# Optimization experiments

Hardware: AMD Instinct MI355X
Metric: run time of the kernel (lower is better)

## Reference

```python
import jax, jax.numpy as jnp
import numpy as np

COMMITMENT_COST = 0.25


def setup_inputs() -> dict:
    key = jax.random.key(0)
    k1, k2 = jax.random.split(key)
    n_embeddings, embedding_dim = 1024, 256
    x = jax.random.normal(k1, (32, 2048, embedding_dim), dtype=jnp.float32)
    r = 1.0 / n_embeddings
    embedding = jax.random.uniform(k2, (n_embeddings, embedding_dim),
                                   dtype=jnp.float32, minval=-r, maxval=r)
    return {"x": x, "embedding": embedding}


def reference(x, embedding):
    M, D = embedding.shape
    # x is detached before flattening in the original quantize()
    x_flat = jax.lax.stop_gradient(x).reshape(-1, D)  # [N, D]
    distances = (jnp.sum(embedding * embedding, axis=1)
                 + jnp.sum(x_flat * x_flat, axis=1, keepdims=True)
                 - 2.0 * (x_flat @ embedding.T))  # [N, M]
    indices = jnp.argmin(distances, axis=-1)  # [N] int
    quantized = embedding[indices].reshape(x.shape)  # gather + view_as(x)
    # commitment loss: quantized is detached in the loss term
    e_latent_loss = jnp.mean(jnp.square(x - jax.lax.stop_gradient(quantized)))
    loss = COMMITMENT_COST * e_latent_loss
    return quantized, loss, indices
```

## Files before the change

kernel.cpp:

```cpp
#include <hip/hip_runtime.h>

#define N_ROWS   65536
#define D        256
#define D4       64
#define M        1024
#define LOSS_OFF 16777216
#define IDX_OFF  16777217
#define COMMIT_SCALE (0.25f / 16777216.0f)
#define E_SCALE  1024.0f
#define C_SCALE  0.001953125f

typedef _Float16 f16x8 __attribute__((ext_vector_type(8)));
typedef _Float16 f16x4 __attribute__((ext_vector_type(4)));
typedef float    f32x4 __attribute__((ext_vector_type(4)));

__device__ __forceinline__ float np_block128(const float* __restrict__ a, int l) {
    float r0 = __fmul_rn(a[l +   0], a[l +   0]);
    float r1 = __fmul_rn(a[l +  16], a[l +  16]);
    float r2 = __fmul_rn(a[l +  32], a[l +  32]);
    float r3 = __fmul_rn(a[l +  48], a[l +  48]);
    float r4 = __fmul_rn(a[l +  64], a[l +  64]);
    float r5 = __fmul_rn(a[l +  80], a[l +  80]);
    float r6 = __fmul_rn(a[l +  96], a[l +  96]);
    float r7 = __fmul_rn(a[l + 112], a[l + 112]);
    return __fadd_rn(__fadd_rn(__fadd_rn(r0, r1), __fadd_rn(r2, r3)),
                     __fadd_rn(__fadd_rn(r4, r5), __fadd_rn(r6, r7)));
}
__device__ __forceinline__ float np_reduce16(float v) {
    float s = __fadd_rn(v, __shfl_down(v, 8));
    s = __fadd_rn(s, __shfl_down(s, 4));
    s = __fadd_rn(s, __shfl_down(s, 2));
    s = __fadd_rn(s, __shfl_down(s, 1));
    return s;
}

__global__ __launch_bounds__(256) void norms_kernel(
    const float* __restrict__ x, const float* __restrict__ emb,
    float* __restrict__ bsq, float* __restrict__ esq,
    float* __restrict__ loss_slot) {
    const int tid = threadIdx.x;
    const int l = tid & 15, g = tid >> 4;
    const float* src;
    float* dst;
    if (blockIdx.x < 4096) {
        const int row = blockIdx.x * 16 + g;
        src = x + (size_t)row * D;
        dst = bsq + row;
    } else {
        const int row = (blockIdx.x - 4096) * 16 + g;
        src = emb + (size_t)row * D;
        dst = esq + row;
    }
    const float v0 = np_block128(src, l);
    const float v1 = np_block128(src + 128, l);
    const float t0 = np_reduce16(v0);
    const float t1 = np_reduce16(v1);
    if (l == 0) *dst = __fadd_rn(t0, t1);
    if (blockIdx.x == 0 && tid == 0) *loss_slot = 0.0f;
}

__global__ __launch_bounds__(256) void esplit_kernel(
    const float4* __restrict__ emb4,
    _Float16* __restrict__ e_hi, _Float16* __restrict__ e_mid) {
    const int f = blockIdx.x * 256 + threadIdx.x;
    float4 v = emb4[f];
    float a[4] = {v.x * E_SCALE, v.y * E_SCALE, v.z * E_SCALE, v.w * E_SCALE};
    f16x4 hi, mid;
    #pragma unroll
    for (int j = 0; j < 4; ++j) {
        _Float16 h = (_Float16)a[j];
        float r = __fsub_rn(a[j], (float)h);
        hi[j] = h;
        mid[j] = (_Float16)r;
    }
    *(f16x4*)&e_hi[f * 4]  = hi;
    *(f16x4*)&e_mid[f * 4] = mid;
}

__global__ __launch_bounds__(256, 2) void argmin_mfma_kernel(
    const float* __restrict__ x,
    const _Float16* __restrict__ e_hi, const _Float16* __restrict__ e_mid,
    const float* __restrict__ esq, const float* __restrict__ bsq,
    float* __restrict__ idx_out_f, int* __restrict__ idx_out_i) {
    __shared__ _Float16 bs[2][128 * 40];
    __shared__ float red_d[64][2];
    __shared__ int   red_i[64][2];

    const int tid = threadIdx.x;
    const int w = tid >> 6, lane = tid & 63;
    const int w_row = w >> 1, w_col = w & 1;
    const int lm = lane & 15, q = lane >> 4;
    const int row0 = blockIdx.x * 64;

    f16x8 a_hi[2][8], a_mid[2][8];
    #pragma unroll
    for (int fm = 0; fm < 2; ++fm) {
        const float* xr = x + (size_t)(row0 + w_row * 32 + fm * 16 + lm) * D + q * 8;
        #pragma unroll
        for (int kc = 0; kc < 8; ++kc) {
            float4 v0 = *(const float4*)(xr + kc * 32);
            float4 v1 = *(const float4*)(xr + kc * 32 + 4);
            float e[8] = {v0.x, v0.y, v0.z, v0.w, v1.x, v1.y, v1.z, v1.w};
            #pragma unroll
            for (int j = 0; j < 8; ++j) {
                _Float16 h = (_Float16)e[j];
                float r = __fsub_rn(e[j], (float)h);
                a_hi[fm][kc][j]  = h;
                a_mid[fm][kc][j] = (_Float16)r;
            }
        }
    }
    float bq[2][4];
    #pragma unroll
    for (int fm = 0; fm < 2; ++fm)
        #pragma unroll
        for (int r = 0; r < 4; ++r)
            bq[fm][r] = bsq[row0 + w_row * 32 + fm * 16 + q * 4 + r];

    float best[2][4] = {{3.0e38f, 3.0e38f, 3.0e38f, 3.0e38f},
                        {3.0e38f, 3.0e38f, 3.0e38f, 3.0e38f}};
    int bidx[2][4] = {{0, 0, 0, 0}, {0, 0, 0, 0}};

    const int sc = tid >> 1;
    const int sh = tid & 1;

    for (int jt = 0; jt < 8; ++jt) {
        const int j0 = jt * 128;
        f32x4 acc[2][4] = {};
        #pragma unroll
        for (int kc = 0; kc < 8; ++kc) {
            __syncthreads();
            const size_t gofs = (size_t)(j0 + sc) * D + kc * 32 + sh * 16;
            _Float16* dh = &bs[0][sc * 40 + sh * 16];
            _Float16* dm = &bs[1][sc * 40 + sh * 16];
            *(uint4*)(dh)     = *(const uint4*)(e_hi + gofs);
            *(uint4*)(dh + 8) = *(const uint4*)(e_hi + gofs + 8);
            *(uint4*)(dm)     = *(const uint4*)(e_mid + gofs);
            *(uint4*)(dm + 8) = *(const uint4*)(e_mid + gofs + 8);
            __syncthreads();
            f16x8 bh[4], bm[4];
            #pragma unroll
            for (int fn = 0; fn < 4; ++fn) {
                const int bo = (w_col * 64 + fn * 16 + lm) * 40 + q * 8;
                bh[fn] = *(const f16x8*)&bs[0][bo];
                bm[fn] = *(const f16x8*)&bs[1][bo];
            }
            #pragma unroll
            for (int fm = 0; fm < 2; ++fm)
                #pragma unroll
                for (int fn = 0; fn < 4; ++fn) {
                    acc[fm][fn] = __builtin_amdgcn_mfma_f32_16x16x32_f16(
                        a_hi[fm][kc], bh[fn], acc[fm][fn], 0, 0, 0);
                    acc[fm][fn] = __builtin_amdgcn_mfma_f32_16x16x32_f16(
                        a_mid[fm][kc], bh[fn], acc[fm][fn], 0, 0, 0);
                    acc[fm][fn] = __builtin_amdgcn_mfma_f32_16x16x32_f16(
                        a_hi[fm][kc], bm[fn], acc[fm][fn], 0, 0, 0);
                }
        }
        #pragma unroll
        for (int fn = 0; fn < 4; ++fn) {
            const int j = j0 + w_col * 64 + fn * 16 + lm;
            const float eq = esq[j];
            #pragma unroll
            for (int fm = 0; fm < 2; ++fm)
                #pragma unroll
                for (int r = 0; r < 4; ++r) {
                    const float d = __fsub_rn(__fadd_rn(eq, bq[fm][r]),
                                              acc[fm][fn][r] * C_SCALE);
                    if (d < best[fm][r]) { best[fm][r] = d; bidx[fm][r] = j; }
                }
        }
    }
    #pragma unroll
    for (int fm = 0; fm < 2; ++fm)
        #pragma unroll
        for (int r = 0; r < 4; ++r) {
            float d = best[fm][r]; int i = bidx[fm][r];
            #pragma unroll
            for (int mv = 1; mv <= 8; mv <<= 1) {
                const float d2 = __shfl_xor(d, mv, 64);
                const int   i2 = __shfl_xor(i, mv, 64);
                if (d2 < d || (d2 == d && i2 < i)) { d = d2; i = i2; }
            }
            best[fm][r] = d; bidx[fm][r] = i;
        }
    __syncthreads();
    if (lm == 0) {
        #pragma unroll
        for (int fm = 0; fm < 2; ++fm)
            #pragma unroll
            for (int r = 0; r < 4; ++r) {
                const int rl = w_row * 32 + fm * 16 + q * 4 + r;
                red_d[rl][w_col] = best[fm][r];
                red_i[rl][w_col] = bidx[fm][r];
            }
    }
    __syncthreads();
    if (tid < 64) {
        float d0 = red_d[tid][0]; int i0 = red_i[tid][0];
        const float d1 = red_d[tid][1]; const int i1 = red_i[tid][1];
        if (d1 < d0 || (d1 == d0 && i1 < i0)) { d0 = d1; i0 = i1; }
        idx_out_f[row0 + tid] = (float)i0;
        idx_out_i[row0 + tid] = i0;
    }
}

__global__ __launch_bounds__(256) void gather_loss_kernel(
    const float4* __restrict__ x4, const float4* __restrict__ emb4,
    const int* __restrict__ idx, float4* __restrict__ q4,
    float* __restrict__ loss_slot) {
    const int base = blockIdx.x * 256 + threadIdx.x;
    float acc = 0.0f;
    #pragma unroll
    for (int i = 0; i < 16; ++i) {
        const int f   = base + i * (1024 * 256);
        const int row = f >> 6;
        const int c4  = f & 63;
        const int e   = idx[row];
        float4 qv = emb4[e * D4 + c4];
        float4 xv = x4[f];
        q4[f] = qv;
        const float dx = xv.x - qv.x, dy = xv.y - qv.y;
        const float dz = xv.z - qv.z, dw = xv.w - qv.w;
        acc += dx * dx + dy * dy + dz * dz + dw * dw;
    }
    #pragma unroll
    for (int off = 32; off; off >>= 1) acc += __shfl_down(acc, off, 64);
    __shared__ float wsum[4];
    const int lane = threadIdx.x & 63, w = threadIdx.x >> 6;
    if (lane == 0) wsum[w] = acc;
    __syncthreads();
    if (threadIdx.x == 0) {
        atomicAdd(loss_slot, (wsum[0] + wsum[1] + wsum[2] + wsum[3]) * COMMIT_SCALE);
    }
}

extern "C" void kernel_launch(void* const* d_in, const int* in_sizes, int n_in,
                              void* d_out, int out_size, void* d_ws, size_t ws_size,
                              hipStream_t stream) {
    const float* x   = (const float*)d_in[0];
    const float* emb = (const float*)d_in[1];
    float* out = (float*)d_out;
    float*    bsq  = (float*)d_ws;
    float*    esq  = bsq + N_ROWS;
    int*      idx  = (int*)(esq + M);
    _Float16* e_hi = (_Float16*)(idx + N_ROWS);
    _Float16* e_mid = e_hi + (size_t)M * D;

    norms_kernel<<<4096 + M / 16, 256, 0, stream>>>(x, emb, bsq, esq,
                                                    out + LOSS_OFF);
    esplit_kernel<<<M * D / 4 / 256, 256, 0, stream>>>((const float4*)emb,
                                                       e_hi, e_mid);
    argmin_mfma_kernel<<<N_ROWS / 64, 256, 0, stream>>>(x, e_hi, e_mid,
                                                        esq, bsq,
                                                        out + IDX_OFF, idx);
    gather_loss_kernel<<<1024, 256, 0, stream>>>((const float4*)x,
                                                 (const float4*)emb, idx,
                                                 (float4*)out, out + LOSS_OFF);
}
```

Before: 253.5 us.

## Double-buffer codebook tiles via async global-to-LDS loads and stage norm rows in LDS

The fp16 hi/mid codebook split is now written in a kc-major tiled layout. This lets each 128-code by 32-dim tile be copied into LDS with contiguous global_load_lds DMA. The argmin kernel double-buffers these tiles and prefetches the next one while MFMAs run on the current one, which removes one barrier per step and the register round-trip of the staging copy. The norms kernel now loads 16 rows with coalesced float4 reads into padded shared memory before doing the same fixed-order reduction. Risks: the unpadded 32-half LDS row stride may cause bank conflicts, and correctness relies on the barrier waiting for the async LDS writes to complete.

```diff
diff --git a/kernel.cpp b/kernel.cpp
--- a/kernel.cpp
+++ b/kernel.cpp
@@ -13,6 +13,12 @@
 typedef _Float16 f16x8 __attribute__((ext_vector_type(8)));
 typedef _Float16 f16x4 __attribute__((ext_vector_type(4)));
 typedef float    f32x4 __attribute__((ext_vector_type(4)));
+
+__device__ __forceinline__ void async_copy16(const void* g, void* l) {
+    __builtin_amdgcn_global_load_lds(
+        (const __attribute__((address_space(1))) unsigned int*)g,
+        (__attribute__((address_space(3))) unsigned int*)l, 16, 0, 0);
+}
 
 __device__ __forceinline__ float np_block128(const float* __restrict__ a, int l) {
     float r0 = __fmul_rn(a[l +   0], a[l +   0]);
@@ -35,27 +41,37 @@
 }
 
 __global__ __launch_bounds__(256) void norms_kernel(
-    const float* __restrict__ x, const float* __restrict__ emb,
+    const float4* __restrict__ x4, const float4* __restrict__ emb4,
     float* __restrict__ bsq, float* __restrict__ esq,
     float* __restrict__ loss_slot) {
+    __shared__ float rowbuf[16 * 260];
     const int tid = threadIdx.x;
+    const float4* src4;
+    float* dst;
+    int row0;
+    if (blockIdx.x < 4096) {
+        row0 = blockIdx.x * 16;
+        src4 = x4 + (size_t)row0 * 64;
+        dst = bsq + row0;
+    } else {
+        row0 = (blockIdx.x - 4096) * 16;
+        src4 = emb4 + (size_t)row0 * 64;
+        dst = esq + row0;
+    }
+    #pragma unroll
+    for (int p = 0; p < 4; ++p) {
+        const int f = tid + p * 256;
+        const int r = f >> 6, c4 = f & 63;
+        *(float4*)&rowbuf[r * 260 + c4 * 4] = src4[f];
+    }
+    __syncthreads();
     const int l = tid & 15, g = tid >> 4;
-    const float* src;
-    float* dst;
-    if (blockIdx.x < 4096) {
-        const int row = blockIdx.x * 16 + g;
-        src = x + (size_t)row * D;
-        dst = bsq + row;
-    } else {
-        const int row = (blockIdx.x - 4096) * 16 + g;
-        src = emb + (size_t)row * D;
-        dst = esq + row;
-    }
-    const float v0 = np_block128(src, l);
-    const float v1 = np_block128(src + 128, l);
+    const float* base = &rowbuf[g * 260];
+    const float v0 = np_block128(base, l);
+    const float v1 = np_block128(base + 128, l);
     const float t0 = np_reduce16(v0);
     const float t1 = np_reduce16(v1);
-    if (l == 0) *dst = __fadd_rn(t0, t1);
+    if (l == 0) dst[g] = __fadd_rn(t0, t1);
     if (blockIdx.x == 0 && tid == 0) *loss_slot = 0.0f;
 }
 
@@ -63,6 +79,8 @@
     const float4* __restrict__ emb4,
     _Float16* __restrict__ e_hi, _Float16* __restrict__ e_mid) {
     const int f = blockIdx.x * 256 + threadIdx.x;
+    const int code = f >> 6, k4 = f & 63;
+    const int kc = k4 >> 3, ko = (k4 & 7) * 4;
     float4 v = emb4[f];
     float a[4] = {v.x * E_SCALE, v.y * E_SCALE, v.z * E_SCALE, v.w * E_SCALE};
     f16x4 hi, mid;
@@ -73,8 +91,9 @@
         hi[j] = h;
         mid[j] = (_Float16)r;
     }
-    *(f16x4*)&e_hi[f * 4]  = hi;
-    *(f16x4*)&e_mid[f * 4] = mid;
+    const size_t ofs = (size_t)kc * (M * 32) + (size_t)code * 32 + ko;
+    *(f16x4*)&e_hi[ofs]  = hi;
+    *(f16x4*)&e_mid[ofs] = mid;
 }
 
 __global__ __launch_bounds__(256, 2) void argmin_mfma_kernel(
@@ -82,7 +101,7 @@
     const _Float16* __restrict__ e_hi, const _Float16* __restrict__ e_mid,
     const float* __restrict__ esq, const float* __restrict__ bsq,
     float* __restrict__ idx_out_f, int* __restrict__ idx_out_i) {
-    __shared__ _Float16 bs[2][128 * 40];
+    __shared__ __attribute__((aligned(16))) _Float16 buf[2][8192];
     __shared__ float red_d[64][2];
     __shared__ int   red_i[64][2];
 
@@ -121,29 +140,35 @@
                         {3.0e38f, 3.0e38f, 3.0e38f, 3.0e38f}};
     int bidx[2][4] = {{0, 0, 0, 0}, {0, 0, 0, 0}};
 
-    const int sc = tid >> 1;
-    const int sh = tid & 1;
-
+    auto dma = [&](int c, int bsel) {
+        const int jt = c >> 3, kc = c & 7;
+        const size_t gofs = (size_t)kc * 65536 + (size_t)jt * 8192
+                          + (size_t)w * 2048 + (size_t)lane * 16;
+        const char* gh = (const char*)e_hi + gofs;
+        const char* gm = (const char*)e_mid + gofs;
+        _Float16* lh = &buf[bsel][w * 1024];
+        _Float16* lmm = &buf[bsel][4096 + w * 1024];
+        async_copy16(gh, lh);
+        async_copy16(gh + 1024, lh + 512);
+        async_copy16(gm, lmm);
+        async_copy16(gm + 1024, lmm + 512);
+    };
+
+    dma(0, 0);
     for (int jt = 0; jt < 8; ++jt) {
         const int j0 = jt * 128;
         f32x4 acc[2][4] = {};
-        #pragma unroll
         for (int kc = 0; kc < 8; ++kc) {
+            const int c = jt * 8 + kc;
             __syncthreads();
-            const size_t gofs = (size_t)(j0 + sc) * D + kc * 32 + sh * 16;
-            _Float16* dh = &bs[0][sc * 40 + sh * 16];
-            _Float16* dm = &bs[1][sc * 40 + sh * 16];
-            *(uint4*)(dh)     = *(const uint4*)(e_hi + gofs);
-            *(uint4*)(dh + 8) = *(const uint4*)(e_hi + gofs + 8);
-            *(uint4*)(dm)     = *(const uint4*)(e_mid + gofs);
-            *(uint4*)(dm + 8) = *(const uint4*)(e_mid + gofs + 8);
-            __syncthreads();
+            if (c < 63) dma(c + 1, (c + 1) & 1);
+            const int bsel = c & 1;
             f16x8 bh[4], bm[4];
             #pragma unroll
             for (int fn = 0; fn < 4; ++fn) {
-                const int bo = (w_col * 64 + fn * 16 + lm) * 40 + q * 8;
-                bh[fn] = *(const f16x8*)&bs[0][bo];
-                bm[fn] = *(const f16x8*)&bs[1][bo];
+                const int bo = (w_col * 64 + fn * 16 + lm) * 32 + q * 8;
+                bh[fn] = *(const f16x8*)&buf[bsel][bo];
+                bm[fn] = *(const f16x8*)&buf[bsel][4096 + bo];
             }
             #pragma unroll
             for (int fm = 0; fm < 2; ++fm)
@@ -247,8 +272,9 @@
     _Float16* e_hi = (_Float16*)(idx + N_ROWS);
     _Float16* e_mid = e_hi + (size_t)M * D;
 
-    norms_kernel<<<4096 + M / 16, 256, 0, stream>>>(x, emb, bsq, esq,
-                                                    out + LOSS_OFF);
+    norms_kernel<<<4096 + M / 16, 256, 0, stream>>>((const float4*)x,
+                                                    (const float4*)emb,
+                                                    bsq, esq, out + LOSS_OFF);
     esplit_kernel<<<M * D / 4 / 256, 256, 0, stream>>>((const float4*)emb,
                                                        e_hi, e_mid);
     argmin_mfma_kernel<<<N_ROWS / 64, 256, 0, stream>>>(x, e_hi, e_mid,
```

After: 251.2 us. No clear change (-0.9%).
